# Performance work log

Measured on AMD Instinct MI355X. Metric: run time of the kernel, lower is better.

## Reference

```python
import jax, jax.numpy as jnp
import numpy as np

B, T, D = 2, 2048, 2048
H, KV = 16, 4
HD = D // H            # 128
REP = H // KV          # 4 query heads per kv head


def setup_inputs() -> dict:
    key = jax.random.key(0)
    ks = jax.random.split(key, 5)
    scale = D ** -0.5
    x = jax.random.normal(ks[0], (B, T, D), dtype=jnp.float32)
    Wq = jax.random.normal(ks[1], (D, H * HD), dtype=jnp.float32) * scale
    Wk = jax.random.normal(ks[2], (D, KV * HD), dtype=jnp.float32) * scale
    Wv = jax.random.normal(ks[3], (D, KV * HD), dtype=jnp.float32) * scale
    Wo = jax.random.normal(ks[4], (H * HD, D), dtype=jnp.float32) * scale
    return {"x": x, "Wq": Wq, "Wk": Wk, "Wv": Wv, "Wo": Wo}


def reference(x, Wq, Wk, Wv, Wo):
    b, t, d = x.shape
    # projections; group query heads by their kv head (repeat_interleave order:
    # q head h uses kv head h // REP, i.e. heads are contiguous per group)
    q = (x @ Wq).reshape(b, t, KV, REP, HD)          # bt(g r)d -> b t g r d
    k = (x @ Wk).reshape(b, t, KV, HD)
    v = (x @ Wv).reshape(b, t, KV, HD)
    # scores: [B, KV, REP, T, T] -- equivalent to repeat_interleave of kv heads
    scores = jnp.einsum('btgrd,bsgd->bgrts', q, k) * (HD ** -0.5)
    causal = jnp.tril(jnp.ones((t, t), dtype=bool))
    scores = jnp.where(causal, scores, -jnp.inf)
    weights = jax.nn.softmax(scores, axis=-1)
    out = jnp.einsum('bgrts,bsgd->btgrd', weights, v).reshape(b, t, H * HD)
    return jnp.round(out @ Wo, decimals=4)
```

## Files before the change

### kernel.cpp

```cpp
#include <hip/hip_runtime.h>
#include <hip/hip_bf16.h>
#include <math.h>

#define B_ 2
#define T_ 2048
#define D_ 2048
#define H_ 16
#define KV_ 4
#define HD_ 128
#define REP_ 4
#define QKVSTR 3072

typedef __attribute__((ext_vector_type(8))) short s16x8;
typedef __attribute__((ext_vector_type(4))) short s16x4;
typedef __attribute__((ext_vector_type(4))) float f32x4;
typedef __attribute__((ext_vector_type(16))) float f32x16;
typedef __hip_bfloat16 bf16;

__device__ __forceinline__ short f2bf(float x) {
    bf16 h = __float2bfloat16(x);
    return *reinterpret_cast<short*>(&h);
}

__device__ __forceinline__ void gl2lds16(const void* g, void* l) {
    __builtin_amdgcn_global_load_lds(
        (const __attribute__((address_space(1))) char*)g,
        (__attribute__((address_space(3))) char*)l, 16, 0, 0);
}

__global__ __launch_bounds__(256) void prep(const float* __restrict__ x,
                                            const float* __restrict__ Wq,
                                            const float* __restrict__ Wk,
                                            const float* __restrict__ Wv,
                                            const float* __restrict__ Wo,
                                            bf16* __restrict__ xb,
                                            bf16* __restrict__ Wqkvt,
                                            bf16* __restrict__ Wot,
                                            float qscale) {
    const int bid = blockIdx.x;
    const int t = threadIdx.x;
    if (bid < 4096) {
        int i = (bid * 256 + t) * 8;
        float4 a = *(const float4*)(x + i);
        float4 b = *(const float4*)(x + i + 4);
        short o[8] = {f2bf(a.x), f2bf(a.y), f2bf(a.z), f2bf(a.w),
                      f2bf(b.x), f2bf(b.y), f2bf(b.z), f2bf(b.w)};
        *(s16x8*)(xb + i) = *(const s16x8*)o;
        return;
    }
    __shared__ unsigned tileT[64 * 33];
    const float* W; bf16* dst; int N; float scale; int seg;
    if (bid < 5120)      { seg = bid - 4096; W = Wq; dst = Wqkvt;                      N = 2048; scale = qscale; }
    else if (bid < 5376) { seg = bid - 5120; W = Wk; dst = Wqkvt + (size_t)2048 * D_;  N = 512;  scale = 1.f; }
    else if (bid < 5632) { seg = bid - 5376; W = Wv; dst = Wqkvt + (size_t)2560 * D_;  N = 512;  scale = 1.f; }
    else                 { seg = bid - 5632; W = Wo; dst = Wot;                        N = 2048; scale = 1.f; }
    const int k0 = (seg & 31) * 64, n0 = (seg >> 5) * 64;

    const int r2 = t >> 3;
    const int c0 = (t & 7) * 8;
    const float* srcA = W + (size_t)(k0 + 2 * r2) * N + n0 + c0;
    const float* srcB = srcA + N;
    float4 a0 = *(const float4*)(srcA);
    float4 a1 = *(const float4*)(srcA + 4);
    float4 b0 = *(const float4*)(srcB);
    float4 b1 = *(const float4*)(srcB + 4);
    float ra[8] = {a0.x, a0.y, a0.z, a0.w, a1.x, a1.y, a1.z, a1.w};
    float rb[8] = {b0.x, b0.y, b0.z, b0.w, b1.x, b1.y, b1.z, b1.w};
    #pragma unroll
    for (int j = 0; j < 8; ++j) {
        unsigned p;
        asm("v_cvt_pk_bf16_f32 %0, %1, %2"
            : "=v"(p) : "v"(ra[j] * scale), "v"(rb[j] * scale));
        tileT[(c0 + j) * 33 + r2] = p;
    }
    __syncthreads();
    const int n = t >> 2, q = t & 3;
    union { unsigned u[8]; s16x8 v[2]; } ou;
    #pragma unroll
    for (int j = 0; j < 8; ++j) ou.u[j] = tileT[n * 33 + q * 8 + j];
    bf16* d = dst + (size_t)(n0 + n) * D_ + k0 + q * 16;
    *(s16x8*)(d)     = ou.v[0];
    *(s16x8*)(d + 8) = ou.v[1];
}

template<int MI, int NJ, typename OUTT, int ROUND, int WVT>
__global__ __launch_bounds__(512, 2) void gemm8(const bf16* __restrict__ A,
                                                const bf16* __restrict__ Bt,
                                                OUTT* __restrict__ C,
                                                bf16* __restrict__ Vtg,
                                                int M, int N, int K) {
    constexpr int ASZ = MI * 2048;
    constexpr int BSZ = NJ * 4096;
    __shared__ short smem[2 * (ASZ + BSZ)];
    const int tid = threadIdx.x;
    const int lane = tid & 63;
    const int wave = tid >> 6;
    const int quad = lane >> 4;
    const int l16 = lane & 15;
    const int wr = wave >> 2, wc = wave & 3;
    const int row0 = blockIdx.y * (MI * 32);
    const int col0 = blockIdx.x * (NJ * 64);
    const int NT = K >> 6;

    f32x4 acc[MI][NJ] = {};

    const bf16* Ap = A + (size_t)row0 * K;
    const bf16* Bp = Bt + (size_t)col0 * K;

    auto stage = [&](int t) {
        const int bo = (t & 1) * (ASZ + BSZ);
        const int k0 = t * 64;
        #pragma unroll
        for (int i = 0; i < MI / 2; ++i) {
            int g = i * 512 + tid;
            int row = g >> 3;
            int cs = (g & 7) ^ (row & 7);
            gl2lds16(Ap + (size_t)row * K + k0 + cs * 8, &smem[bo + g * 8]);
        }
        #pragma unroll
        for (int i = 0; i < NJ; ++i) {
            int g = i * 512 + tid;
            int row = g >> 3;
            int cs = (g & 7) ^ (row & 7);
            gl2lds16(Bp + (size_t)row * K + k0 + cs * 8, &smem[bo + ASZ + g * 8]);
        }
    };

    constexpr int VM = MI / 2 + NJ;
    static_assert(VM == 6 || VM == 7, "add a vmcnt literal for this shape");

    stage(0);
    for (int t = 0; t < NT; ++t) {
        if (t + 1 < NT) {
            stage(t + 1);
            if constexpr (VM == 7) asm volatile("s_waitcnt vmcnt(7)" ::: "memory");
            else                   asm volatile("s_waitcnt vmcnt(6)" ::: "memory");
        } else {
            asm volatile("s_waitcnt vmcnt(0)" ::: "memory");
        }
        __builtin_amdgcn_s_barrier();
        asm volatile("" ::: "memory");

        const int bo = (t & 1) * (ASZ + BSZ);
        #pragma unroll
        for (int kk = 0; kk < 2; ++kk) {
            s16x8 af[MI], bfr[NJ];
            #pragma unroll
            for (int i = 0; i < MI; ++i) {
                int row = wr * (MI * 16) + i * 16 + l16;
                int c = (kk * 4 + quad) ^ (row & 7);
                af[i] = *(const s16x8*)&smem[bo + row * 64 + c * 8];
            }
            #pragma unroll
            for (int j = 0; j < NJ; ++j) {
                int row = wc * (NJ * 16) + j * 16 + l16;
                int c = (kk * 4 + quad) ^ (row & 7);
                bfr[j] = *(const s16x8*)&smem[bo + ASZ + row * 64 + c * 8];
            }
            __builtin_amdgcn_s_setprio(1);
            #pragma unroll
            for (int i = 0; i < MI; ++i)
                #pragma unroll
                for (int j = 0; j < NJ; ++j)
                    acc[i][j] = __builtin_amdgcn_mfma_f32_16x16x32_bf16(
                        af[i], bfr[j], acc[i][j], 0, 0, 0);
            __builtin_amdgcn_s_setprio(0);
        }
        asm volatile("s_waitcnt lgkmcnt(0)" ::: "memory");
        __builtin_amdgcn_s_barrier();
        asm volatile("" ::: "memory");
    }

    #pragma unroll
    for (int i = 0; i < MI; ++i) {
        #pragma unroll
        for (int j = 0; j < NJ; ++j) {
            const int col = col0 + wc * (NJ * 16) + j * 16 + l16;
            const int rowb = row0 + wr * (MI * 16) + i * 16 + quad * 4;
            #pragma unroll
            for (int r = 0; r < 4; ++r) {
                float v = acc[i][j][r];
                if (ROUND) v = rintf(v * 1e4f) * 1e-4f;
                if constexpr (sizeof(OUTT) == 2)
                    C[(size_t)(rowb + r) * N + col] = __float2bfloat16(v);
                else
                    C[(size_t)(rowb + r) * N + col] = v;
            }
            if constexpr (WVT) {
                if (col >= 2560) {
                    const int dcol = (col - 2560) & 127;
                    const int g = (col - 2560) >> 7;
                    const int b = rowb >> 11;
                    const int t = rowb & 2047;
                    short pk[4] = {f2bf(acc[i][j][0]), f2bf(acc[i][j][1]),
                                   f2bf(acc[i][j][2]), f2bf(acc[i][j][3])};
                    *(s16x4*)&Vtg[(size_t)((b * KV_ + g) * HD_ + dcol) * T_ + t] =
                        *(const s16x4*)pk;
                }
            }
        }
    }
}

__global__ __launch_bounds__(256, 2) void flash9(const bf16* __restrict__ Q,
                                                 const bf16* __restrict__ K,
                                                 const bf16* __restrict__ Vtg,
                                                 bf16* __restrict__ O) {
    __shared__ short smem[32768];

    const int h = blockIdx.x;
    const int b = blockIdx.y & 1;
    const int qt = 15 - (blockIdx.y >> 1);
    const int g = h >> 2;
    const int tid = threadIdx.x;
    const int lane = tid & 63;
    const int wave = tid >> 6;
    const int l32 = lane & 31;
    const int hi = lane >> 5;
    const int qw0 = qt * 128 + wave * 32;
    const int qg = qw0 + l32;

    s16x8 qf[8];
    {
        const bf16* qp = Q + (size_t)(b * T_ + qg) * QKVSTR + h * HD_ + hi * 8;
        #pragma unroll
        for (int kt = 0; kt < 8; ++kt) qf[kt] = *(const s16x8*)(qp + kt * 16);
    }

    const bf16* Kp = K + (size_t)(b * T_) * QKVSTR + g * HD_;
    const bf16* Vp = Vtg + (size_t)((b * KV_ + g) * HD_) * T_;

    float l_part = 0.f;
    f32x16 oacc[4] = {};

    const int jmax = 2 * qt + 1;

    #pragma unroll
    for (int i = 0; i < 4; ++i) {
        int g2 = i * 256 + tid;
        int s = g2 >> 4;
        int cs = (g2 & 15) ^ (s & 15);
        gl2lds16(Kp + (size_t)s * QKVSTR + cs * 8, &smem[g2 * 8]);
    }
    #pragma unroll
    for (int i = 0; i < 4; ++i) {
        int g2 = i * 256 + tid;
        int d = g2 >> 3;
        int cs = (g2 & 7) ^ (d & 7);
        gl2lds16(Vp + (size_t)d * T_ + cs * 8, &smem[8192 + g2 * 8]);
    }

    for (int j = 0; j <= jmax; ++j) {
        const int kb = (j & 1) << 14;
        __syncthreads();

        if (j < jmax) {
            const int s0n = (j + 1) * 64;
            const int nb = ((j + 1) & 1) << 14;
            #pragma unroll
            for (int i = 0; i < 4; ++i) {
                int g2 = i * 256 + tid;
                int s = g2 >> 4;
                int cs = (g2 & 15) ^ (s & 15);
                gl2lds16(Kp + (size_t)(s0n + s) * QKVSTR + cs * 8, &smem[nb + g2 * 8]);
            }
            #pragma unroll
            for (int i = 0; i < 4; ++i) {
                int g2 = i * 256 + tid;
                int d = g2 >> 3;
                int cs = (g2 & 7) ^ (d & 7);
                gl2lds16(Vp + (size_t)d * T_ + s0n + cs * 8, &smem[nb + 8192 + g2 * 8]);
            }
        }

        const int s0 = j * 64;
        if (s0 >= qw0 + 32) continue;

        f32x16 sacc[2] = {};
        #pragma unroll
        for (int kt = 0; kt < 8; ++kt) {
            #pragma unroll
            for (int mt = 0; mt < 2; ++mt) {
                int s = mt * 32 + l32;
                int c = (kt * 2 + hi) ^ (s & 15);
                const s16x8 kf = *(const s16x8*)&smem[kb + s * 128 + c * 8];
                sacc[mt] = __builtin_amdgcn_mfma_f32_32x32x16_bf16(
                    kf, qf[kt], sacc[mt], 0, 0, 0);
            }
        }

        const bool diagw = (s0 + 63 > qw0);
        #pragma unroll
        for (int mt = 0; mt < 2; ++mt) {
            #pragma unroll
            for (int r = 0; r < 16; ++r) {
                float sv = sacc[mt][r];
                if (diagw) {
                    int sg = s0 + mt * 32 + (r & 3) + 8 * (r >> 2) + 4 * hi;
                    if (sg > qg) sv = -INFINITY;
                }
                float e = exp2f(sv);
                sacc[mt][r] = e;
                l_part += e;
            }
            #pragma unroll
            for (int kts = 0; kts < 2; ++kts) {
                const int o = kts * 8;
                unsigned w01, w23, w45, w67;
                asm("v_cvt_pk_bf16_f32 %0, %1, %2"
                    : "=v"(w01) : "v"(sacc[mt][o + 0]), "v"(sacc[mt][o + 1]));
                asm("v_cvt_pk_bf16_f32 %0, %1, %2"
                    : "=v"(w23) : "v"(sacc[mt][o + 2]), "v"(sacc[mt][o + 3]));
                asm("v_cvt_pk_bf16_f32 %0, %1, %2"
                    : "=v"(w45) : "v"(sacc[mt][o + 4]), "v"(sacc[mt][o + 5]));
                asm("v_cvt_pk_bf16_f32 %0, %1, %2"
                    : "=v"(w67) : "v"(sacc[mt][o + 6]), "v"(sacc[mt][o + 7]));
                asm("v_permlane32_swap_b32 %0, %1" : "+v"(w01), "+v"(w45));
                asm("v_permlane32_swap_b32 %0, %1" : "+v"(w23), "+v"(w67));
                union { unsigned u[4]; s16x8 v; } pu;
                pu.u[0] = w01; pu.u[1] = w23; pu.u[2] = w45; pu.u[3] = w67;
                const s16x8 pa = pu.v;
                #pragma unroll
                for (int nt = 0; nt < 4; ++nt) {
                    int d = nt * 32 + l32;
                    int c = ((mt * 2 + kts) * 2 + hi) ^ (d & 7);
                    const s16x8 vf = *(const s16x8*)&smem[kb + 8192 + d * 64 + c * 8];
                    oacc[nt] = __builtin_amdgcn_mfma_f32_32x32x16_bf16(
                        pa, vf, oacc[nt], 0, 0, 0);
                }
            }
        }
    }

    l_part += __shfl_xor(l_part, 32);
    const float invl = 1.f / l_part;

    bf16* op = O + (size_t)(b * T_ + qw0) * (H_ * HD_) + h * HD_;
    #pragma unroll
    for (int r = 0; r < 16; ++r) {
        const int qrow = (r & 3) + 8 * (r >> 2) + 4 * hi;
        const float il = __shfl(invl, qrow);
        #pragma unroll
        for (int nt = 0; nt < 4; ++nt)
            op[(size_t)qrow * (H_ * HD_) + nt * 32 + l32] =
                __float2bfloat16(oacc[nt][r] * il);
    }
}

extern "C" void kernel_launch(void* const* d_in, const int* in_sizes, int n_in,
                              void* d_out, int out_size, void* d_ws, size_t ws_size,
                              hipStream_t stream) {
    const float* x  = (const float*)d_in[0];
    const float* Wq = (const float*)d_in[1];
    const float* Wk = (const float*)d_in[2];
    const float* Wv = (const float*)d_in[3];
    const float* Wo = (const float*)d_in[4];
    float* out = (float*)d_out;

    const size_t NR = (size_t)B_ * T_;
    bf16* ws = (bf16*)d_ws;
    bf16* xb    = ws;
    bf16* Wqkvt = xb + NR * D_;
    bf16* Wot   = Wqkvt + (size_t)QKVSTR * D_;
    bf16* QKVb  = Wot + (size_t)D_ * D_;
    bf16* Vtg   = QKVb + NR * QKVSTR;
    bf16* Ab    = Vtg + (size_t)B_ * KV_ * HD_ * T_;

    const float qscale = 1.4426950408889634f / sqrtf((float)HD_);

    prep<<<6656, 256, 0, stream>>>(x, Wq, Wk, Wv, Wo, xb, Wqkvt, Wot, qscale);

    gemm8<8, 3, bf16, 0, 1><<<dim3(QKVSTR / 192, NR / 256), 512, 0, stream>>>(
        xb, Wqkvt, QKVb, Vtg, (int)NR, QKVSTR, D_);

    flash9<<<dim3(H_, 32), 256, 0, stream>>>(QKVb, QKVb + 2048, Vtg, Ab);

    gemm8<4, 4, float, 1, 0><<<dim3(D_ / 256, NR / 128), 512, 0, stream>>>(
        Ab, Wot, out, nullptr, (int)NR, D_, H_ * HD_);
}
```

Measured before the change: 274.4 us.

## Software-pipeline flash attention: overlap QK^T of next tile with softmax·V of previous

Restructures the attention loop so each iteration computes QK^T scores for tile t while applying exp and the PV MFMA for tile t-1. The single K buffer and a three-slot V ring replace the old double-buffered K/V. A mid-iteration barrier decides when the next K tile may be staged. The causal skip moves from per-wave to per-32-row subtile granularity. The aim is to interleave MFMA and exp/convert work and hide load latency, at the cost of two extra barriers per tile and more live registers for two score accumulators.

```diff
diff --git a/kernel.cpp b/kernel.cpp
--- a/kernel.cpp
+++ b/kernel.cpp
@@ -202,10 +202,10 @@
     }
 }
 
-__global__ __launch_bounds__(256, 2) void flash9(const bf16* __restrict__ Q,
-                                                 const bf16* __restrict__ K,
-                                                 const bf16* __restrict__ Vtg,
-                                                 bf16* __restrict__ O) {
+__global__ __launch_bounds__(256, 2) void flash11(const bf16* __restrict__ Q,
+                                                  const bf16* __restrict__ K,
+                                                  const bf16* __restrict__ Vtg,
+                                                  bf16* __restrict__ O) {
     __shared__ short smem[32768];
 
     const int h = blockIdx.x;
@@ -232,75 +232,46 @@
 
     float l_part = 0.f;
     f32x16 oacc[4] = {};
+    f32x16 sA[2], sB[2];
 
     const int jmax = 2 * qt + 1;
 
-    #pragma unroll
-    for (int i = 0; i < 4; ++i) {
-        int g2 = i * 256 + tid;
-        int s = g2 >> 4;
-        int cs = (g2 & 15) ^ (s & 15);
-        gl2lds16(Kp + (size_t)s * QKVSTR + cs * 8, &smem[g2 * 8]);
-    }
-    #pragma unroll
-    for (int i = 0; i < 4; ++i) {
-        int g2 = i * 256 + tid;
-        int d = g2 >> 3;
-        int cs = (g2 & 7) ^ (d & 7);
-        gl2lds16(Vp + (size_t)d * T_ + cs * 8, &smem[8192 + g2 * 8]);
-    }
-
-    for (int j = 0; j <= jmax; ++j) {
-        const int kb = (j & 1) << 14;
-        __syncthreads();
-
-        if (j < jmax) {
-            const int s0n = (j + 1) * 64;
-            const int nb = ((j + 1) & 1) << 14;
-            #pragma unroll
-            for (int i = 0; i < 4; ++i) {
-                int g2 = i * 256 + tid;
-                int s = g2 >> 4;
-                int cs = (g2 & 15) ^ (s & 15);
-                gl2lds16(Kp + (size_t)(s0n + s) * QKVSTR + cs * 8, &smem[nb + g2 * 8]);
-            }
-            #pragma unroll
-            for (int i = 0; i < 4; ++i) {
-                int g2 = i * 256 + tid;
-                int d = g2 >> 3;
-                int cs = (g2 & 7) ^ (d & 7);
-                gl2lds16(Vp + (size_t)d * T_ + s0n + cs * 8, &smem[nb + 8192 + g2 * 8]);
-            }
-        }
-
-        const int s0 = j * 64;
-        if (s0 >= qw0 + 32) continue;
-
-        f32x16 sacc[2] = {};
-        #pragma unroll
-        for (int kt = 0; kt < 8; ++kt) {
-            #pragma unroll
-            for (int mt = 0; mt < 2; ++mt) {
-                int s = mt * 32 + l32;
-                int c = (kt * 2 + hi) ^ (s & 15);
-                const s16x8 kf = *(const s16x8*)&smem[kb + s * 128 + c * 8];
-                sacc[mt] = __builtin_amdgcn_mfma_f32_32x32x16_bf16(
-                    kf, qf[kt], sacc[mt], 0, 0, 0);
-            }
-        }
-
-        const bool diagw = (s0 + 63 > qw0);
+    auto stageK = [&](int t) {
+        const int s0n = t * 64;
+        #pragma unroll
+        for (int i = 0; i < 4; ++i) {
+            int g2 = i * 256 + tid;
+            int s = g2 >> 4;
+            int cs = (g2 & 15) ^ (s & 15);
+            gl2lds16(Kp + (size_t)(s0n + s) * QKVSTR + cs * 8, &smem[g2 * 8]);
+        }
+    };
+    auto stageV = [&](int t, int slot) {
+        const int s0n = t * 64;
+        #pragma unroll
+        for (int i = 0; i < 4; ++i) {
+            int g2 = i * 256 + tid;
+            int d = g2 >> 3;
+            int cs = (g2 & 7) ^ (d & 7);
+            gl2lds16(Vp + (size_t)d * T_ + s0n + cs * 8,
+                     &smem[8192 + slot * 8192 + g2 * 8]);
+        }
+    };
+
+    auto smpv = [&](int s0p, f32x16* prv, int vslot) {
         #pragma unroll
         for (int mt = 0; mt < 2; ++mt) {
+            if (s0p + mt * 32 >= qw0 + 32) continue;
+            const bool diagm = (s0p + mt * 32 + 31 > qw0);
             #pragma unroll
             for (int r = 0; r < 16; ++r) {
-                float sv = sacc[mt][r];
-                if (diagw) {
-                    int sg = s0 + mt * 32 + (r & 3) + 8 * (r >> 2) + 4 * hi;
+                float sv = prv[mt][r];
+                if (diagm) {
+                    int sg = s0p + mt * 32 + (r & 3) + 8 * (r >> 2) + 4 * hi;
                     if (sg > qg) sv = -INFINITY;
                 }
                 float e = exp2f(sv);
-                sacc[mt][r] = e;
+                prv[mt][r] = e;
                 l_part += e;
             }
             #pragma unroll
@@ -308,13 +279,13 @@
                 const int o = kts * 8;
                 unsigned w01, w23, w45, w67;
                 asm("v_cvt_pk_bf16_f32 %0, %1, %2"
-                    : "=v"(w01) : "v"(sacc[mt][o + 0]), "v"(sacc[mt][o + 1]));
+                    : "=v"(w01) : "v"(prv[mt][o + 0]), "v"(prv[mt][o + 1]));
                 asm("v_cvt_pk_bf16_f32 %0, %1, %2"
-                    : "=v"(w23) : "v"(sacc[mt][o + 2]), "v"(sacc[mt][o + 3]));
+                    : "=v"(w23) : "v"(prv[mt][o + 2]), "v"(prv[mt][o + 3]));
                 asm("v_cvt_pk_bf16_f32 %0, %1, %2"
-                    : "=v"(w45) : "v"(sacc[mt][o + 4]), "v"(sacc[mt][o + 5]));
+                    : "=v"(w45) : "v"(prv[mt][o + 4]), "v"(prv[mt][o + 5]));
                 asm("v_cvt_pk_bf16_f32 %0, %1, %2"
-                    : "=v"(w67) : "v"(sacc[mt][o + 6]), "v"(sacc[mt][o + 7]));
+                    : "=v"(w67) : "v"(prv[mt][o + 6]), "v"(prv[mt][o + 7]));
                 asm("v_permlane32_swap_b32 %0, %1" : "+v"(w01), "+v"(w45));
                 asm("v_permlane32_swap_b32 %0, %1" : "+v"(w23), "+v"(w67));
                 union { unsigned u[4]; s16x8 v; } pu;
@@ -324,12 +295,56 @@
                 for (int nt = 0; nt < 4; ++nt) {
                     int d = nt * 32 + l32;
                     int c = ((mt * 2 + kts) * 2 + hi) ^ (d & 7);
-                    const s16x8 vf = *(const s16x8*)&smem[kb + 8192 + d * 64 + c * 8];
+                    const s16x8 vf =
+                        *(const s16x8*)&smem[8192 + vslot * 8192 + d * 64 + c * 8];
                     oacc[nt] = __builtin_amdgcn_mfma_f32_32x32x16_bf16(
                         pa, vf, oacc[nt], 0, 0, 0);
                 }
             }
         }
+    };
+
+    auto tile = [&](int t, f32x16* cur, f32x16* prv, int vprev, int vnext) {
+        __syncthreads();
+        if (t < jmax) stageV(t + 1, vnext);
+        const int s0 = t * 64;
+        if (s0 < qw0 + 32) {
+            #pragma unroll
+            for (int r = 0; r < 16; ++r) { cur[0][r] = 0.f; cur[1][r] = 0.f; }
+            #pragma unroll
+            for (int kt = 0; kt < 8; ++kt) {
+                #pragma unroll
+                for (int mt = 0; mt < 2; ++mt) {
+                    int s = mt * 32 + l32;
+                    int c = (kt * 2 + hi) ^ (s & 15);
+                    const s16x8 kf = *(const s16x8*)&smem[s * 128 + c * 8];
+                    cur[mt] = __builtin_amdgcn_mfma_f32_32x32x16_bf16(
+                        kf, qf[kt], cur[mt], 0, 0, 0);
+                }
+            }
+        }
+        asm volatile("s_waitcnt lgkmcnt(0)" ::: "memory");
+        __builtin_amdgcn_s_barrier();
+        asm volatile("" ::: "memory");
+        if (t < jmax) stageK(t + 1);
+        if (t > 0) smpv(s0 - 64, prv, vprev);
+    };
+
+    stageK(0);
+    stageV(0, 0);
+
+    int v0 = 0;
+    for (int p = 0; p <= qt; ++p) {
+        const int t0 = 2 * p;
+        const int v1 = (v0 + 1 == 3) ? 0 : v0 + 1;
+        const int v2 = (v1 + 1 == 3) ? 0 : v1 + 1;
+        tile(t0,     sA, sB, v2, v1);
+        tile(t0 + 1, sB, sA, v0, v2);
+        v0 = v2;
+    }
+    {
+        int vlast = v0 + 2; if (vlast >= 3) vlast -= 3;
+        smpv(jmax * 64, sB, vlast);
     }
 
     l_part += __shfl_xor(l_part, 32);
@@ -373,7 +388,7 @@
     gemm8<8, 3, bf16, 0, 1><<<dim3(QKVSTR / 192, NR / 256), 512, 0, stream>>>(
         xb, Wqkvt, QKVb, Vtg, (int)NR, QKVSTR, D_);
 
-    flash9<<<dim3(H_, 32), 256, 0, stream>>>(QKVb, QKVb + 2048, Vtg, Ab);
+    flash11<<<dim3(H_, 32), 256, 0, stream>>>(QKVb, QKVb + 2048, Vtg, Ab);
 
     gemm8<4, 4, float, 1, 0><<<dim3(D_ / 256, NR / 128), 512, 0, stream>>>(
         Ab, Wot, out, nullptr, (int)NR, D_, H_ * HD_);
```

After: 277.4 us. Within noise of the previous version (+1.1%).
